# Kernel tuning notes

Hardware: AMD Instinct MI355X
Metric: run time of the kernel (lower is better)

## Reference

```python
import jax, jax.numpy as jnp
import numpy as np

N_NODES = 500_000
N_EDGES = 4_000_000


def setup_inputs() -> dict:
    key = jax.random.key(0)
    k1, k2, k3, k4 = jax.random.split(key, 4)
    x = jax.random.normal(k1, (N_NODES, 3), dtype=jnp.float32)
    edge_index = jax.random.randint(k2, (2, N_EDGES), 0, N_NODES, dtype=jnp.int32)
    # GCNConv(3, 16) and GCNConv(16, 1): weight [in, out], bias [out]
    W1 = jax.random.normal(k3, (3, 16), dtype=jnp.float32) / np.sqrt(3.0)
    b1 = jnp.zeros((16,), dtype=jnp.float32)
    W2 = jax.random.normal(k4, (16, 1), dtype=jnp.float32) / np.sqrt(16.0)
    b2 = jnp.zeros((1,), dtype=jnp.float32)
    return {"x": x, "edge_index": edge_index, "W1": W1, "b1": b1, "W2": W2, "b2": b2}


def gcn_conv(x, edge_index, W, b):
    """PyG GCNConv: add self-loops, symmetric deg^-1/2 normalization,
    linear transform, scatter-add aggregation to target nodes, bias."""
    n = x.shape[0]
    loop = jnp.arange(n, dtype=edge_index.dtype)
    row = jnp.concatenate([edge_index[0], loop])  # source nodes
    col = jnp.concatenate([edge_index[1], loop])  # target nodes
    deg = jax.ops.segment_sum(jnp.ones_like(col, dtype=x.dtype), col, num_segments=n)
    deg_inv_sqrt = jnp.where(deg > 0, jax.lax.rsqrt(jnp.maximum(deg, 1.0)), 0.0)
    norm = deg_inv_sqrt[row] * deg_inv_sqrt[col]  # [E+N]
    h = x @ W  # [N, out]
    msg = h[row] * norm[:, None]  # gather + scale, [E+N, out]
    out = jax.ops.segment_sum(msg, col, num_segments=n)  # scatter-add
    return out + b


def reference(x, edge_index, W1, b1, W2, b2):
    h = jax.nn.relu(gcn_conv(x, edge_index, W1, b1))
    return gcn_conv(h, edge_index, W2, b2)  # [N, 1]
```

## Files before the change

kernel.cpp:

```cpp
#include <hip/hip_runtime.h>
#include <hip/hip_fp16.h>


typedef float vf4 __attribute__((ext_vector_type(4)));

#define NB 512
#define SHIFT 10
#define SLICE 1024
#define CAP 11264
#define P1T 1024
#define P1PER 16
#define P1E (P1T * P1PER)
#define SENT 0xFFFFFFFFu

__global__ __launch_bounds__(1024) void p1_partition(
        const int* __restrict__ row, const int* __restrict__ col,
        unsigned* __restrict__ gcur, unsigned* __restrict__ buf, int E) {
    __shared__ unsigned hist[NB];
    __shared__ unsigned loff[NB], lcur[NB], gbase[NB];
    __shared__ unsigned stage[P1E];
    __shared__ unsigned wsum[16];
    int t = threadIdx.x;
    if (t < NB) hist[t] = 0;
    __syncthreads();
    long long e0 = (long long)blockIdx.x * P1E;
    unsigned ent[P1PER];
    int bkt[P1PER];
#pragma unroll
    for (int j = 0; j < P1PER; j++) {
        long long e = e0 + (long long)j * P1T + t;
        if (e < E) {
            int c = __builtin_nontemporal_load(col + e);
            int r = __builtin_nontemporal_load(row + e);
            ent[j] = ((unsigned)r << SHIFT) | (unsigned)(c & (SLICE - 1));
            bkt[j] = c >> SHIFT;
            atomicAdd(&hist[bkt[j]], 1u);
        } else bkt[j] = -1;
    }
    __syncthreads();
    unsigned myc = 0, v = 0;
    int lane = t & 63, w = t >> 6;
    if (t < NB) {
        myc = hist[t];
        v = myc;
#pragma unroll
        for (int d = 1; d < 64; d <<= 1) {
            unsigned o = __shfl_up(v, d, 64);
            if (lane >= d) v += o;
        }
        if (lane == 63) wsum[w] = v;
    }
    __syncthreads();
    if (w == 0) {
        unsigned s = (lane < 8) ? wsum[lane] : 0u, sv = s;
#pragma unroll
        for (int d = 1; d < 8; d <<= 1) {
            unsigned o = __shfl_up(sv, d, 64);
            if (lane >= d) sv += o;
        }
        if (lane < 8) wsum[lane] = sv - s;
    }
    __syncthreads();
    if (t < NB) {
        unsigned excl = v - myc + wsum[w];
        loff[t] = excl;
        lcur[t] = excl;
        unsigned padded = (myc + 15u) & ~15u;
        gbase[t] = padded ? atomicAdd(&gcur[t], padded) : 0u;
        hist[t] = padded;
    }
    __syncthreads();
#pragma unroll
    for (int j = 0; j < P1PER; j++) {
        if (bkt[j] >= 0) {
            unsigned p = atomicAdd(&lcur[bkt[j]], 1u);
            stage[p] = ent[j];
        }
    }
    __syncthreads();
    if (t < NB) {
        unsigned c = myc, padded = hist[t], lo = loff[t], gb = gbase[t];
        unsigned* dst = buf + (size_t)t * CAP + gb;
        for (unsigned s = 0; s + 4 <= padded && gb + s + 4 <= CAP; s += 4) {
            uint4 q;
            q.x = (s + 0 < c) ? stage[lo + s + 0] : SENT;
            q.y = (s + 1 < c) ? stage[lo + s + 1] : SENT;
            q.z = (s + 2 < c) ? stage[lo + s + 2] : SENT;
            q.w = (s + 3 < c) ? stage[lo + s + 3] : SENT;
            *(uint4*)(dst + s) = q;
        }
    }
}

__global__ __launch_bounds__(1024) void k2a(
        const unsigned* __restrict__ gcur, const unsigned* __restrict__ buf,
        const float* __restrict__ x, float* __restrict__ dis,
        uint2* __restrict__ xs4h, unsigned* __restrict__ pstart,
        unsigned* __restrict__ buf2, int N) {
    __shared__ unsigned sorted[CAP];
    __shared__ unsigned cnts[SLICE];
    __shared__ unsigned pos[SLICE];
    __shared__ unsigned wsum[16];
    __shared__ unsigned stot;
    int b = blockIdx.x, t = threadIdx.x;
    cnts[t] = 0;
    __syncthreads();
    unsigned ext = min(gcur[b], (unsigned)CAP);
    const unsigned* bp = buf + (size_t)b * CAP;
    for (unsigned i = t; i < ext; i += 1024) {
        unsigned e = __builtin_nontemporal_load(bp + i);
        if (e != SENT) atomicAdd(&cnts[e & (SLICE - 1)], 1u);
    }
    __syncthreads();
    unsigned myc = cnts[t];
    unsigned v = myc;
    int lane = t & 63, w = t >> 6;
#pragma unroll
    for (int d = 1; d < 64; d <<= 1) {
        unsigned o = __shfl_up(v, d, 64);
        if (lane >= d) v += o;
    }
    if (lane == 63) wsum[w] = v;
    __syncthreads();
    if (w == 0) {
        unsigned s = (lane < 16) ? wsum[lane] : 0u, sv = s;
#pragma unroll
        for (int d = 1; d < 16; d <<= 1) {
            unsigned o = __shfl_up(sv, d, 64);
            if (lane >= d) sv += o;
        }
        if (lane < 16) wsum[lane] = sv - s;
    }
    __syncthreads();
    unsigned excl = v - myc + wsum[w];
    pos[t] = excl;
    if (t == 1023) stot = excl + myc;
    int c = (b << SHIFT) + t;
    if (c < N) {
        float d = rsqrtf(1.0f + (float)myc);
        dis[c] = d;
        __half2 h01 = __floats2half2_rn(d * x[3 * c], d * x[3 * c + 1]);
        __half2 h23 = __floats2half2_rn(d * x[3 * c + 2], 0.f);
        uint2 u;
        u.x = *(unsigned*)&h01;
        u.y = *(unsigned*)&h23;
        xs4h[c] = u;
        pstart[c] = (excl << 8) | min(myc, 255u);
    }
    __syncthreads();
    for (unsigned i = t; i < ext; i += 1024) {
        unsigned e = __builtin_nontemporal_load(bp + i);
        if (e != SENT) {
            unsigned p = atomicAdd(&pos[e & (SLICE - 1)], 1u);
            sorted[p] = e >> SHIFT;
        }
    }
    __syncthreads();
    unsigned tot = stot;
    unsigned* b2p = buf2 + (size_t)b * CAP;
    for (unsigned i = t; i < tot; i += 1024) b2p[i] = sorted[i];
}

__global__ __launch_bounds__(1024) void k2b(
        const unsigned* __restrict__ pstart, const unsigned* __restrict__ buf2,
        const uint2* __restrict__ xs4h, const float* __restrict__ x,
        const float* __restrict__ dis,
        const float* __restrict__ W1, const float* __restrict__ b1,
        const float* __restrict__ W2, float* __restrict__ hs2, int N) {
    __shared__ float sW[48], sb[16], sw2[16];
    int b = blockIdx.x, t = threadIdx.x;
    if (t < 48) sW[t] = W1[t];
    if (t < 16) { sb[t] = b1[t]; sw2[t] = W2[t]; }
    __syncthreads();
    int c = (b << SHIFT) + t;
    if (c >= N) return;
    unsigned meta = pstart[c];
    const unsigned* sp = buf2 + (size_t)b * CAP + (meta >> 8);
    unsigned cnt = meta & 255u;
    float d = dis[c];
    float a0 = d * x[3 * c], a1 = d * x[3 * c + 1], a2 = d * x[3 * c + 2];
    unsigned j = 0;
    for (; j + 4 <= cnt; j += 4) {
        unsigned r0 = sp[j], r1 = sp[j + 1], r2 = sp[j + 2], r3 = sp[j + 3];
        uint2 u0 = xs4h[r0], u1 = xs4h[r1], u2 = xs4h[r2], u3 = xs4h[r3];
        float2 f0 = __half22float2(*(__half2*)&u0.x); float g0 = __low2float(*(__half2*)&u0.y);
        float2 f1 = __half22float2(*(__half2*)&u1.x); float g1 = __low2float(*(__half2*)&u1.y);
        float2 f2 = __half22float2(*(__half2*)&u2.x); float g2 = __low2float(*(__half2*)&u2.y);
        float2 f3 = __half22float2(*(__half2*)&u3.x); float g3 = __low2float(*(__half2*)&u3.y);
        a0 += (f0.x + f1.x) + (f2.x + f3.x);
        a1 += (f0.y + f1.y) + (f2.y + f3.y);
        a2 += (g0 + g1) + (g2 + g3);
    }
    for (; j < cnt; j++) {
        uint2 u = xs4h[sp[j]];
        float2 f = __half22float2(*(__half2*)&u.x);
        a0 += f.x; a1 += f.y; a2 += __low2float(*(__half2*)&u.y);
    }
    float s = 0.f;
#pragma unroll
    for (int k = 0; k < 16; k++) {
        float z = fmaxf(d * (a0 * sW[k] + a1 * sW[16 + k] + a2 * sW[32 + k]) + sb[k], 0.f);
        s += z * sw2[k];
    }
    hs2[c] = d * s;
}

__global__ __launch_bounds__(1024) void k2c(
        const unsigned* __restrict__ pstart, const unsigned* __restrict__ buf2,
        const float* __restrict__ hs2, const float* __restrict__ dis,
        const float* __restrict__ b2, float* __restrict__ out, int N) {
    int b = blockIdx.x, t = threadIdx.x;
    int c = (b << SHIFT) + t;
    if (c >= N) return;
    unsigned meta = pstart[c];
    const unsigned* sp = buf2 + (size_t)b * CAP + (meta >> 8);
    unsigned cnt = meta & 255u;
    float s = hs2[c];
    unsigned j = 0;
    for (; j + 4 <= cnt; j += 4) {
        unsigned r0 = sp[j], r1 = sp[j + 1], r2 = sp[j + 2], r3 = sp[j + 3];
        float v0 = hs2[r0], v1 = hs2[r1], v2 = hs2[r2], v3 = hs2[r3];
        s += (v0 + v1) + (v2 + v3);
    }
    for (; j < cnt; j++) s += hs2[sp[j]];
    out[c] = dis[c] * s + b2[0];
}

__global__ void fb_deg(const int* __restrict__ col, float* __restrict__ deg, int E) {
    int e = blockIdx.x * blockDim.x + threadIdx.x;
    if (e < E) atomicAdd(&deg[col[e]], 1.0f);
}
__global__ void fb_pass_a(const float* __restrict__ x, const float* __restrict__ deg,
                          float* __restrict__ dis, vf4* __restrict__ xs4, int N) {
    int i = blockIdx.x * blockDim.x + threadIdx.x;
    if (i >= N) return;
    float d = rsqrtf(deg[i] + 1.0f);
    dis[i] = d;
    vf4 v; v.x = d * x[3 * i]; v.y = d * x[3 * i + 1]; v.z = d * x[3 * i + 2]; v.w = 0.f;
    xs4[i] = v;
}
__global__ void fb_aggx(const int* __restrict__ ei, const float* __restrict__ xs4,
                        float* __restrict__ accx, int E) {
    int t = blockIdx.x * blockDim.x + threadIdx.x;
    int e = t >> 2, k = t & 3;
    if (e >= E) return;
    int r = ei[e], c = ei[E + e];
    float val = xs4[4 * r + k];
    if (k < 3) atomicAdd(&accx[4 * c + k], val);
}
__global__ void fb_post1(const vf4* __restrict__ accx, const vf4* __restrict__ xs4,
                         const float* __restrict__ dis, const float* __restrict__ W1,
                         const float* __restrict__ b1, const float* __restrict__ W2,
                         float* __restrict__ hs2, int N) {
    __shared__ float sW[48], sb[16], sw2[16];
    if (threadIdx.x < 48) sW[threadIdx.x] = W1[threadIdx.x];
    if (threadIdx.x < 16) { sb[threadIdx.x] = b1[threadIdx.x]; sw2[threadIdx.x] = W2[threadIdx.x]; }
    __syncthreads();
    int i = blockIdx.x * blockDim.x + threadIdx.x;
    if (i >= N) return;
    vf4 a = accx[i], self = xs4[i];
    float a0 = a.x + self.x, a1 = a.y + self.y, a2 = a.z + self.z;
    float d = dis[i], s = 0.f;
#pragma unroll
    for (int k = 0; k < 16; k++) {
        float z = fmaxf(d * (a0 * sW[k] + a1 * sW[16 + k] + a2 * sW[32 + k]) + sb[k], 0.f);
        s += z * sw2[k];
    }
    hs2[i] = d * s;
}
__global__ void fb_agg2(const int* __restrict__ ei, const float* __restrict__ hs2,
                        float* __restrict__ acc2, int E) {
    int e = blockIdx.x * blockDim.x + threadIdx.x;
    if (e >= E) return;
    atomicAdd(&acc2[ei[E + e]], hs2[ei[e]]);
}
__global__ void fb_fin(const float* __restrict__ acc2, const float* __restrict__ hs2,
                       const float* __restrict__ dis, const float* __restrict__ b2,
                       float* __restrict__ out, int N) {
    int i = blockIdx.x * blockDim.x + threadIdx.x;
    if (i < N) out[i] = dis[i] * (acc2[i] + hs2[i]) + b2[0];
}

extern "C" void kernel_launch(void* const* d_in, const int* in_sizes, int n_in,
                              void* d_out, int out_size, void* d_ws, size_t ws_size,
                              hipStream_t stream) {
    const float* x  = (const float*)d_in[0];
    const int*   ei = (const int*)d_in[1];
    const float* W1 = (const float*)d_in[2];
    const float* b1 = (const float*)d_in[3];
    const float* W2 = (const float*)d_in[4];
    const float* b2 = (const float*)d_in[5];
    float* out = (float*)d_out;

    const int N = in_sizes[0] / 3;
    const int E = in_sizes[1] / 2;
    const int* row = ei;
    const int* col = ei + E;

    float* ws = (float*)d_ws;
    size_t need = (size_t)(1024 + 2 * (size_t)NB * CAP + 5 * (size_t)N) * 4;

    if (ws_size >= need) {
        unsigned* gcur = (unsigned*)ws;
        unsigned* buf  = (unsigned*)ws + 1024;
        unsigned* buf2 = buf + (size_t)NB * CAP;
        float* dis  = (float*)(buf2 + (size_t)NB * CAP);
        uint2* xs4h = (uint2*)(dis + N);
        float* hs2  = dis + 3 * (size_t)N;
        unsigned* pstart = (unsigned*)(dis + 4 * (size_t)N);

        hipMemsetAsync(gcur, 0, 1024 * sizeof(unsigned), stream);
        int p1g = (E + P1E - 1) / P1E;
        p1_partition<<<p1g, P1T, 0, stream>>>(row, col, gcur, buf, E);
        k2a<<<NB, 1024, 0, stream>>>(gcur, buf, x, dis, xs4h, pstart, buf2, N);
        k2b<<<NB, 1024, 0, stream>>>(pstart, buf2, xs4h, x, dis, W1, b1, W2, hs2, N);
        k2c<<<NB, 1024, 0, stream>>>(pstart, buf2, hs2, dis, b2, out, N);
    } else {
        float* deg = ws;
        float* dis = ws + (size_t)N;
        vf4*  xs4 = (vf4*)(ws + 2 * (size_t)N);
        float* accx = ws + 6 * (size_t)N;
        float* hs2 = ws + 10 * (size_t)N;
        float* acc2 = ws + 11 * (size_t)N;
        const int B = 256;
        hipMemsetAsync(deg, 0, (size_t)N * sizeof(float), stream);
        hipMemsetAsync(accx, 0, 4 * (size_t)N * sizeof(float), stream);
        hipMemsetAsync(acc2, 0, (size_t)N * sizeof(float), stream);
        fb_deg<<<(E + B - 1) / B, B, 0, stream>>>(col, deg, E);
        fb_pass_a<<<(N + B - 1) / B, B, 0, stream>>>(x, deg, dis, xs4, N);
        long long t4 = (long long)E * 4;
        fb_aggx<<<(int)((t4 + B - 1) / B), B, 0, stream>>>(ei, (const float*)xs4, accx, E);
        fb_post1<<<(N + B - 1) / B, B, 0, stream>>>((const vf4*)accx, xs4, dis, W1, b1, W2, hs2, N);
        fb_agg2<<<(E + B - 1) / B, B, 0, stream>>>(ei, hs2, acc2, E);
        fb_fin<<<(N + B - 1) / B, B, 0, stream>>>(acc2, hs2, dis, b2, out, N);
    }
}
```

Before: 177.9 us.

## Fuse sort, layer-1 and layer-2 kernels into persistent kernel with grid barriers

```diff
diff --git a/kernel.cpp b/kernel.cpp
--- a/kernel.cpp
+++ b/kernel.cpp
@@ -92,17 +92,21 @@
     }
 }
 
-__global__ __launch_bounds__(1024) void k2a(
+__global__ __launch_bounds__(1024, 8) void k2fused(
         const unsigned* __restrict__ gcur, const unsigned* __restrict__ buf,
-        const float* __restrict__ x, float* __restrict__ dis,
-        uint2* __restrict__ xs4h, unsigned* __restrict__ pstart,
-        unsigned* __restrict__ buf2, int N) {
+        const float* __restrict__ x,
+        const float* __restrict__ W1, const float* __restrict__ b1,
+        const float* __restrict__ W2, const float* __restrict__ b2,
+        unsigned long long* __restrict__ xs4h, float* __restrict__ hs2,
+        float* __restrict__ out, unsigned* __restrict__ bar, int N) {
     __shared__ unsigned sorted[CAP];
     __shared__ unsigned cnts[SLICE];
     __shared__ unsigned pos[SLICE];
     __shared__ unsigned wsum[16];
-    __shared__ unsigned stot;
+    __shared__ float sW[48], sb[16], sw2[16];
     int b = blockIdx.x, t = threadIdx.x;
+    if (t < 48) sW[t] = W1[t];
+    if (t < 16) { sb[t] = b1[t]; sw2[t] = W2[t]; }
     cnts[t] = 0;
     __syncthreads();
     unsigned ext = min(gcur[b], (unsigned)CAP);
@@ -134,18 +138,16 @@
     __syncthreads();
     unsigned excl = v - myc + wsum[w];
     pos[t] = excl;
-    if (t == 1023) stot = excl + myc;
     int c = (b << SHIFT) + t;
+    float d = 0.f, a0s = 0.f, a1s = 0.f, a2s = 0.f;
     if (c < N) {
-        float d = rsqrtf(1.0f + (float)myc);
-        dis[c] = d;
-        __half2 h01 = __floats2half2_rn(d * x[3 * c], d * x[3 * c + 1]);
-        __half2 h23 = __floats2half2_rn(d * x[3 * c + 2], 0.f);
-        uint2 u;
-        u.x = *(unsigned*)&h01;
-        u.y = *(unsigned*)&h23;
-        xs4h[c] = u;
-        pstart[c] = (excl << 8) | min(myc, 255u);
+        d = rsqrtf(1.0f + (float)myc);
+        a0s = d * x[3 * c]; a1s = d * x[3 * c + 1]; a2s = d * x[3 * c + 2];
+        __half2 h01 = __floats2half2_rn(a0s, a1s);
+        __half2 h23 = __floats2half2_rn(a2s, 0.f);
+        unsigned lohw = *(unsigned*)&h01, hihw = *(unsigned*)&h23;
+        unsigned long long u = ((unsigned long long)hihw << 32) | lohw;
+        __hip_atomic_store(&xs4h[c], u, __ATOMIC_RELAXED, __HIP_MEMORY_SCOPE_AGENT);
     }
     __syncthreads();
     for (unsigned i = t; i < ext; i += 1024) {
@@ -156,74 +158,74 @@
         }
     }
     __syncthreads();
-    unsigned tot = stot;
-    unsigned* b2p = buf2 + (size_t)b * CAP;
-    for (unsigned i = t; i < tot; i += 1024) b2p[i] = sorted[i];
-}
-
-__global__ __launch_bounds__(1024) void k2b(
-        const unsigned* __restrict__ pstart, const unsigned* __restrict__ buf2,
-        const uint2* __restrict__ xs4h, const float* __restrict__ x,
-        const float* __restrict__ dis,
-        const float* __restrict__ W1, const float* __restrict__ b1,
-        const float* __restrict__ W2, float* __restrict__ hs2, int N) {
-    __shared__ float sW[48], sb[16], sw2[16];
-    int b = blockIdx.x, t = threadIdx.x;
-    if (t < 48) sW[t] = W1[t];
-    if (t < 16) { sb[t] = b1[t]; sw2[t] = W2[t]; }
-    __syncthreads();
-    int c = (b << SHIFT) + t;
-    if (c >= N) return;
-    unsigned meta = pstart[c];
-    const unsigned* sp = buf2 + (size_t)b * CAP + (meta >> 8);
-    unsigned cnt = meta & 255u;
-    float d = dis[c];
-    float a0 = d * x[3 * c], a1 = d * x[3 * c + 1], a2 = d * x[3 * c + 2];
-    unsigned j = 0;
-    for (; j + 4 <= cnt; j += 4) {
-        unsigned r0 = sp[j], r1 = sp[j + 1], r2 = sp[j + 2], r3 = sp[j + 3];
-        uint2 u0 = xs4h[r0], u1 = xs4h[r1], u2 = xs4h[r2], u3 = xs4h[r3];
-        float2 f0 = __half22float2(*(__half2*)&u0.x); float g0 = __low2float(*(__half2*)&u0.y);
-        float2 f1 = __half22float2(*(__half2*)&u1.x); float g1 = __low2float(*(__half2*)&u1.y);
-        float2 f2 = __half22float2(*(__half2*)&u2.x); float g2 = __low2float(*(__half2*)&u2.y);
-        float2 f3 = __half22float2(*(__half2*)&u3.x); float g3 = __low2float(*(__half2*)&u3.y);
-        a0 += (f0.x + f1.x) + (f2.x + f3.x);
-        a1 += (f0.y + f1.y) + (f2.y + f3.y);
-        a2 += (g0 + g1) + (g2 + g3);
-    }
-    for (; j < cnt; j++) {
-        uint2 u = xs4h[sp[j]];
-        float2 f = __half22float2(*(__half2*)&u.x);
-        a0 += f.x; a1 += f.y; a2 += __low2float(*(__half2*)&u.y);
-    }
-    float s = 0.f;
-#pragma unroll
-    for (int k = 0; k < 16; k++) {
-        float z = fmaxf(d * (a0 * sW[k] + a1 * sW[16 + k] + a2 * sW[32 + k]) + sb[k], 0.f);
-        s += z * sw2[k];
-    }
-    hs2[c] = d * s;
-}
-
-__global__ __launch_bounds__(1024) void k2c(
-        const unsigned* __restrict__ pstart, const unsigned* __restrict__ buf2,
-        const float* __restrict__ hs2, const float* __restrict__ dis,
-        const float* __restrict__ b2, float* __restrict__ out, int N) {
-    int b = blockIdx.x, t = threadIdx.x;
-    int c = (b << SHIFT) + t;
-    if (c >= N) return;
-    unsigned meta = pstart[c];
-    const unsigned* sp = buf2 + (size_t)b * CAP + (meta >> 8);
-    unsigned cnt = meta & 255u;
-    float s = hs2[c];
-    unsigned j = 0;
-    for (; j + 4 <= cnt; j += 4) {
-        unsigned r0 = sp[j], r1 = sp[j + 1], r2 = sp[j + 2], r3 = sp[j + 3];
-        float v0 = hs2[r0], v1 = hs2[r1], v2 = hs2[r2], v3 = hs2[r3];
-        s += (v0 + v1) + (v2 + v3);
-    }
-    for (; j < cnt; j++) s += hs2[sp[j]];
-    out[c] = dis[c] * s + b2[0];
+    if (t == 0) {
+        __threadfence();
+        atomicAdd(&bar[0], 1u);
+        while (__hip_atomic_load(&bar[0], __ATOMIC_RELAXED,
+                                 __HIP_MEMORY_SCOPE_AGENT) < (unsigned)gridDim.x)
+            __builtin_amdgcn_s_sleep(8);
+        __threadfence();
+    }
+    __syncthreads();
+
+    float h = 0.f;
+    if (c < N) {
+        float a0 = a0s, a1 = a1s, a2 = a2s;
+        unsigned j = excl, end = excl + myc;
+        for (; j + 4 <= end; j += 4) {
+            unsigned r0 = sorted[j], r1 = sorted[j + 1];
+            unsigned r2 = sorted[j + 2], r3 = sorted[j + 3];
+            unsigned long long u0 = xs4h[r0], u1 = xs4h[r1];
+            unsigned long long u2 = xs4h[r2], u3 = xs4h[r3];
+            unsigned l0 = (unsigned)u0, h0 = (unsigned)(u0 >> 32);
+            unsigned l1 = (unsigned)u1, h1 = (unsigned)(u1 >> 32);
+            unsigned l2 = (unsigned)u2, h2 = (unsigned)(u2 >> 32);
+            unsigned l3 = (unsigned)u3, h3 = (unsigned)(u3 >> 32);
+            float2 f0 = __half22float2(*(__half2*)&l0); float g0 = __low2float(*(__half2*)&h0);
+            float2 f1 = __half22float2(*(__half2*)&l1); float g1 = __low2float(*(__half2*)&h1);
+            float2 f2 = __half22float2(*(__half2*)&l2); float g2 = __low2float(*(__half2*)&h2);
+            float2 f3 = __half22float2(*(__half2*)&l3); float g3 = __low2float(*(__half2*)&h3);
+            a0 += (f0.x + f1.x) + (f2.x + f3.x);
+            a1 += (f0.y + f1.y) + (f2.y + f3.y);
+            a2 += (g0 + g1) + (g2 + g3);
+        }
+        for (; j < end; j++) {
+            unsigned long long u = xs4h[sorted[j]];
+            unsigned lo = (unsigned)u, hi = (unsigned)(u >> 32);
+            float2 f = __half22float2(*(__half2*)&lo);
+            a0 += f.x; a1 += f.y; a2 += __low2float(*(__half2*)&hi);
+        }
+        float s = 0.f;
+#pragma unroll
+        for (int k = 0; k < 16; k++) {
+            float z = fmaxf(d * (a0 * sW[k] + a1 * sW[16 + k] + a2 * sW[32 + k]) + sb[k], 0.f);
+            s += z * sw2[k];
+        }
+        h = d * s;
+        __hip_atomic_store(&hs2[c], h, __ATOMIC_RELAXED, __HIP_MEMORY_SCOPE_AGENT);
+    }
+    __syncthreads();
+    if (t == 0) {
+        __threadfence();
+        atomicAdd(&bar[1], 1u);
+        while (__hip_atomic_load(&bar[1], __ATOMIC_RELAXED,
+                                 __HIP_MEMORY_SCOPE_AGENT) < (unsigned)gridDim.x)
+            __builtin_amdgcn_s_sleep(8);
+        __threadfence();
+    }
+    __syncthreads();
+
+    if (c < N) {
+        float s = h;
+        unsigned j = excl, end = excl + myc;
+        for (; j + 4 <= end; j += 4) {
+            float v0 = hs2[sorted[j]], v1 = hs2[sorted[j + 1]];
+            float v2 = hs2[sorted[j + 2]], v3 = hs2[sorted[j + 3]];
+            s += (v0 + v1) + (v2 + v3);
+        }
+        for (; j < end; j++) s += hs2[sorted[j]];
+        out[c] = d * s + b2[0];
+    }
 }
 
 __global__ void fb_deg(const int* __restrict__ col, float* __restrict__ deg, int E) {
@@ -298,23 +300,20 @@
     const int* col = ei + E;
 
     float* ws = (float*)d_ws;
-    size_t need = (size_t)(1024 + 2 * (size_t)NB * CAP + 5 * (size_t)N) * 4;
+    size_t need = (size_t)(1040 + (size_t)NB * CAP + 3 * (size_t)N) * 4;
 
     if (ws_size >= need) {
         unsigned* gcur = (unsigned*)ws;
-        unsigned* buf  = (unsigned*)ws + 1024;
-        unsigned* buf2 = buf + (size_t)NB * CAP;
-        float* dis  = (float*)(buf2 + (size_t)NB * CAP);
-        uint2* xs4h = (uint2*)(dis + N);
-        float* hs2  = dis + 3 * (size_t)N;
-        unsigned* pstart = (unsigned*)(dis + 4 * (size_t)N);
-
-        hipMemsetAsync(gcur, 0, 1024 * sizeof(unsigned), stream);
+        unsigned* bar  = (unsigned*)ws + 1024;
+        unsigned* buf  = (unsigned*)ws + 1040;
+        unsigned long long* xs4h = (unsigned long long*)(buf + (size_t)NB * CAP);
+        float* hs2  = (float*)(xs4h + N);
+
+        hipMemsetAsync(ws, 0, 1040 * sizeof(unsigned), stream);
         int p1g = (E + P1E - 1) / P1E;
         p1_partition<<<p1g, P1T, 0, stream>>>(row, col, gcur, buf, E);
-        k2a<<<NB, 1024, 0, stream>>>(gcur, buf, x, dis, xs4h, pstart, buf2, N);
-        k2b<<<NB, 1024, 0, stream>>>(pstart, buf2, xs4h, x, dis, W1, b1, W2, hs2, N);
-        k2c<<<NB, 1024, 0, stream>>>(pstart, buf2, hs2, dis, b2, out, N);
+        k2fused<<<NB, 1024, 0, stream>>>(gcur, buf, x, W1, b1, W2, b2,
+                                         xs4h, hs2, out, bar, N);
     } else {
         float* deg = ws;
         float* dis = ws + (size_t)N;
```

After: 281.9 us. +58.5%, slower.
